# Performance work log

Hardware: AMD Instinct MI355X
Metric: run time of the kernel (lower is better)

The kernel has to match this reference:

```python
import jax, jax.numpy as jnp
import numpy as np

VOCAB_SIZE = 512  # matches init_kwargs


def setup_inputs() -> dict:
    key = jax.random.key(0)
    k1, k2, k3 = jax.random.split(key, 3)
    B, S, W = 256, 256, 20
    sents = jax.random.randint(k1, (B, S, W), 0, VOCAB_SIZE, dtype=jnp.int32)
    lengths = jax.random.randint(k2, (B,), 1, S + 1, dtype=jnp.int32)
    forgetting_factor = jax.random.uniform(k3, (1,), dtype=jnp.float32)
    return {"sents": sents, "lengths": lengths, "forgetting_factor": forgetting_factor}


def reference(sents, lengths, forgetting_factor):
    # Original recurrence per word: z = alpha * z + onehot(char_k), k = 0..W-1
    # Closed form: z[v] = sum_k alpha**(W-1-k) * [char_k == v]
    B, S, W = sents.shape
    alpha = forgetting_factor[0]
    # decay weights, oldest char gets highest power: [W]
    exps = jnp.arange(W - 1, -1, -1, dtype=jnp.float32)
    w = alpha ** exps  # [W]
    out = jnp.zeros((B, S, VOCAB_SIZE), dtype=jnp.float32)
    b_idx = jnp.arange(B)[:, None, None]
    s_idx = jnp.arange(S)[None, :, None]
    # scatter-add the decay weight of each char position into its vocab slot
    out = out.at[b_idx, s_idx, sents].add(jnp.broadcast_to(w, (B, S, W)))
    return (out, lengths)
```

## Files before the change

kernel.cpp:

```cpp
#include <hip/hip_runtime.h>
#include <hip/hip_bf16.h>

#define VOCAB 512
#define W 20
#define R 8

typedef float f4 __attribute__((ext_vector_type(4)));

__global__ __launch_bounds__(256) void fofe_kernel(
    const int*   __restrict__ sents,
    const int*   __restrict__ lengths,
    const float* __restrict__ alpha_p,
    float*       __restrict__ out,
    int rows, int B)
{
    __shared__ float lds[R * VOCAB];

    const int tid  = threadIdx.x;
    const int row0 = blockIdx.x * R;

    float w = 0.f;
    int   c = 0;
    int   r = 0;
    if (tid < R * W) {
        r = tid / W;
        const int k = tid - r * W;
        c = sents[(size_t)(row0 + r) * W + k];
        const float alpha = alpha_p[0];
        w = exp2f(log2f(alpha) * (float)(W - 1 - k));
        if (k == W - 1) w = 1.0f;
    }

    f4* l4 = (f4*)lds;
    #pragma unroll
    for (int i = 0; i < 4; ++i)
        l4[tid + 256 * i] = (f4){0.f, 0.f, 0.f, 0.f};

    __syncthreads();

    if (tid < R * W)
        atomicAdd(&lds[r * VOCAB + c], w);

    __syncthreads();

    f4* o4 = (f4*)(out + (size_t)row0 * VOCAB);
    #pragma unroll
    for (int i = 0; i < 4; ++i)
        __builtin_nontemporal_store(l4[tid + 256 * i], &o4[tid + 256 * i]);

    if (blockIdx.x == 0 && tid < B) {
        out[(size_t)rows * VOCAB + tid] = (float)lengths[tid];
    }
}

extern "C" void kernel_launch(void* const* d_in, const int* in_sizes, int n_in,
                              void* d_out, int out_size, void* d_ws, size_t ws_size,
                              hipStream_t stream) {
    const int*   sents   = (const int*)d_in[0];
    const int*   lengths = (const int*)d_in[1];
    const float* alpha   = (const float*)d_in[2];
    float*       out     = (float*)d_out;

    const int rows = in_sizes[0] / W;
    const int B    = in_sizes[1];

    const int blocks = (rows + R - 1) / R;
    fofe_kernel<<<blocks, 256, 0, stream>>>(sents, lengths, alpha, out, rows, B);
}
```

Measured before the change: 144.5 us.

## Replace LDS atomic histogram with wave-shuffle dedup and direct global scatter

Each wave now handles one row. Lanes zero the output tile directly in global memory, then dedupe the row's 20 character indices with wave shuffles, and the first lane holding each distinct index writes the summed weight straight to global. This removes the LDS buffer, the LDS zeroing, the shared-memory atomics and one barrier, and halves rows per block to four. In exchange, the zero stores are ordinary rather than nontemporal, and small scattered stores land on lines that were just written. The launch also assumes the row count divides evenly by four.

New measurement: 149.6 us. 1.04x slower.

```diff
diff --git a/kernel.cpp b/kernel.cpp
--- a/kernel.cpp
+++ b/kernel.cpp
@@ -3,7 +3,7 @@
 
 #define VOCAB 512
 #define W 20
-#define R 8
+#define R 4
 
 typedef float f4 __attribute__((ext_vector_type(4)));
 
@@ -14,42 +14,46 @@
     float*       __restrict__ out,
     int rows, int B)
 {
-    __shared__ float lds[R * VOCAB];
+    const int tid  = threadIdx.x;
+    const int wv   = tid >> 6;
+    const int lane = tid & 63;
+    const int row  = blockIdx.x * R + wv;
+    const bool act = (lane < W);
 
-    const int tid  = threadIdx.x;
-    const int row0 = blockIdx.x * R;
-
+    int   c = -1;
     float w = 0.f;
-    int   c = 0;
-    int   r = 0;
-    if (tid < R * W) {
-        r = tid / W;
-        const int k = tid - r * W;
-        c = sents[(size_t)(row0 + r) * W + k];
+    if (act) {
+        c = sents[(size_t)row * W + lane];
         const float alpha = alpha_p[0];
-        w = exp2f(log2f(alpha) * (float)(W - 1 - k));
-        if (k == W - 1) w = 1.0f;
+        w = (lane == W - 1) ? 1.0f : exp2f(log2f(alpha) * (float)(W - 1 - lane));
     }
 
-    f4* l4 = (f4*)lds;
-    #pragma unroll
-    for (int i = 0; i < 4; ++i)
-        l4[tid + 256 * i] = (f4){0.f, 0.f, 0.f, 0.f};
+    {
+        f4* o4 = (f4*)(out + (size_t)blockIdx.x * R * VOCAB);
+        const f4 z = (f4){0.f, 0.f, 0.f, 0.f};
+        o4[tid]       = z;
+        o4[tid + 256] = z;
+    }
+
+    if (blockIdx.x == 0 && tid < B) {
+        out[(size_t)rows * VOCAB + tid] = (float)lengths[tid];
+    }
 
     __syncthreads();
 
-    if (tid < R * W)
-        atomicAdd(&lds[r * VOCAB + c], w);
-
-    __syncthreads();
-
-    f4* o4 = (f4*)(out + (size_t)row0 * VOCAB);
+    float tot   = 0.f;
+    bool  first = true;
     #pragma unroll
-    for (int i = 0; i < 4; ++i)
-        __builtin_nontemporal_store(l4[tid + 256 * i], &o4[tid + 256 * i]);
-
-    if (blockIdx.x == 0 && tid < B) {
-        out[(size_t)rows * VOCAB + tid] = (float)lengths[tid];
+    for (int j = 0; j < W; ++j) {
+        const int   cj = __shfl(c, j);
+        const float wj = __shfl(w, j);
+        if (cj == c) {
+            tot += wj;
+            if (j < lane) first = false;
+        }
+    }
+    if (act && first) {
+        out[(size_t)row * VOCAB + c] = tot;
     }
 }
 
@@ -64,6 +68,6 @@
     const int rows = in_sizes[0] / W;
     const int B    = in_sizes[1];
 
-    const int blocks = (rows + R - 1) / R;
+    const int blocks = rows / R;
     fofe_kernel<<<blocks, 256, 0, stream>>>(sents, lengths, alpha, out, rows, B);
 }
```
